# Kernel tuning notes

Hardware: AMD Instinct MI355X
Metric: run time of the kernel (lower is better)

Reference implementation:

```python
import jax, jax.numpy as jnp
import numpy as np


def setup_inputs() -> dict:
    key = jax.random.key(0)
    k1, k2 = jax.random.split(key)
    B, N = 2, 8192
    pred = jax.random.normal(k1, (B, N, 3), dtype=jnp.float32)
    gt = jax.random.normal(k2, (B, N, 3), dtype=jnp.float32)
    return {"pred": pred, "gt": gt}


def reference(pred, gt):
    # dist[b, i, j] = ||pred[b, j] - gt[b, i]||_2, computed via the
    # squared-norm expansion to avoid materializing a [B,N,N,3] diff tensor.
    p_sq = jnp.sum(pred * pred, axis=-1)  # [B, N]
    g_sq = jnp.sum(gt * gt, axis=-1)      # [B, N]
    # inner[b, i, j] = gt[b, i] . pred[b, j]
    inner = jnp.einsum("bid,bjd->bij", gt, pred)  # [B, N, N]
    sq_dist = g_sq[:, :, None] + p_sq[:, None, :] - 2.0 * inner
    dist = jnp.sqrt(jnp.maximum(sq_dist, 0.0))    # [B, N, N]
    dist1 = jnp.min(dist, axis=2)  # per-gt nearest pred distance, [B, N]
    dist2 = jnp.min(dist, axis=1)  # per-pred nearest gt distance, [B, N]
    chamfer = (dist1.mean(axis=1) + dist2.mean(axis=1)).mean()
    return chamfer
```

## Files before the change

kernel.cpp:

```cpp
#include <hip/hip_runtime.h>
#include <math.h>

#define NPTS   8192
#define BATCH  2
#define TPB    256
#define PPB    32
#define NBLK   (2 * BATCH * NPTS / PPB)
#define CHUNK  1024
#define NCHUNK (NPTS / CHUNK)
#define NSL    64
#define GPS    (CHUNK / NSL / 4)
#define SPAD   (GPS + 1)
#define KPT    (PPB / 4)
#define POISON 0xAAAAAAAAu
#define TARGET (POISON + (unsigned)NBLK - 1u)
#define SCALE  (1.0f / (float)(BATCH * NPTS))

typedef float v2f __attribute__((ext_vector_type(2)));
typedef float v4f __attribute__((ext_vector_type(4)));

__global__ __launch_bounds__(TPB, 2) void chamfer_fused(
    const float* __restrict__ pred, const float* __restrict__ gt,
    unsigned int* __restrict__ ws, float* __restrict__ out)
{
    __shared__ v4f S[4 * NSL * SPAD];
    __shared__ float psq_l[PPB];
    v4f* xs4 = S;
    v4f* ys4 = S + NSL * SPAD;
    v4f* zs4 = S + 2 * NSL * SPAD;
    v4f* qs4 = S + 3 * NSL * SPAD;

    const int tid = threadIdx.x;
    const int pg  = tid & 3;
    const int cs  = tid >> 2;

    const int base = blockIdx.x * PPB;
    const int dir  = base >> 14;
    const int b    = (base >> 13) & 1;
    const int i0   = base & (NPTS - 1);

    const float* pts  = (dir == 0 ? gt : pred) + (size_t)b * NPTS * 3;
    const float* cand = (dir == 0 ? pred : gt) + (size_t)b * NPTS * 3;

    float px[KPT], py[KPT], pz[KPT], m[KPT];
    {
        const v4f* p4 = (const v4f*)(pts + (size_t)(i0 + pg * KPT) * 3);
        v4f A0 = p4[0], A1 = p4[1], A2 = p4[2], A3 = p4[3], A4 = p4[4], A5 = p4[5];
        px[0] = A0.x; py[0] = A0.y; pz[0] = A0.z;
        px[1] = A0.w; py[1] = A1.x; pz[1] = A1.y;
        px[2] = A1.z; py[2] = A1.w; pz[2] = A2.x;
        px[3] = A2.y; py[3] = A2.z; pz[3] = A2.w;
        px[4] = A3.x; py[4] = A3.y; pz[4] = A3.z;
        px[5] = A3.w; py[5] = A4.x; pz[5] = A4.y;
        px[6] = A4.z; py[6] = A4.w; pz[6] = A5.x;
        px[7] = A5.y; py[7] = A5.z; pz[7] = A5.w;
#pragma unroll
        for (int k = 0; k < KPT; ++k) m[k] = 3.0e38f;
    }

    const v4f* cand4 = (const v4f*)cand;

    for (int c = 0; c < NCHUNK; ++c) {
        if (c) __syncthreads();
        {
            const v4f* cb = cand4 + (size_t)c * (CHUNK * 3 / 4);
            v4f a  = cb[tid * 3 + 0];
            v4f bb = cb[tid * 3 + 1];
            v4f cc = cb[tid * 3 + 2];
            v4f X = {a.x, a.w, bb.z, cc.y};
            v4f Y = {a.y, bb.x, bb.w, cc.z};
            v4f Z = {a.z, bb.y, cc.x, cc.w};
            v4f Q = 0.5f * (X * X + Y * Y + Z * Z);
            int idx = (tid >> 2) * SPAD + (tid & 3);
            xs4[idx] = X; ys4[idx] = Y; zs4[idx] = Z; qs4[idx] = Q;
        }
        __syncthreads();

#pragma unroll
        for (int g = 0; g < GPS; ++g) {
            int idx = cs * SPAD + g;
            v4f cx = xs4[idx], cy = ys4[idx], cz = zs4[idx], cq = qs4[idx];
            v2f cxa = cx.xy, cxb = cx.zw, cya = cy.xy, cyb = cy.zw;
            v2f cza = cz.xy, czb = cz.zw, cqa = cq.xy, cqb = cq.zw;
#pragma unroll
            for (int k = 0; k < KPT; ++k) {
                v2f ta = cqa - cxa * px[k];
                ta = ta - cya * py[k];
                ta = ta - cza * pz[k];
                v2f tb = cqb - cxb * px[k];
                tb = tb - cyb * py[k];
                tb = tb - czb * pz[k];
                m[k] = fminf(fminf(m[k], ta.x), ta.y);
                m[k] = fminf(fminf(m[k], tb.x), tb.y);
            }
        }
    }

    __syncthreads();
    float* pl = (float*)S;
#pragma unroll
    for (int k = 0; k < KPT; ++k)
        pl[(pg * KPT + k) * 68 + cs] = m[k];
    if (cs == 0) {
#pragma unroll
        for (int k = 0; k < KPT; ++k)
            psq_l[pg * KPT + k] = fmaf(px[k], px[k], fmaf(py[k], py[k], pz[k] * pz[k]));
    }
    __syncthreads();

    if (tid < PPB) {
        const v4f* pm4 = (const v4f*)pl;
        v4f mv = pm4[tid * 17];
#pragma unroll
        for (int j = 1; j < 16; ++j) {
            v4f t = pm4[tid * 17 + j];
            mv.x = fminf(mv.x, t.x); mv.y = fminf(mv.y, t.y);
            mv.z = fminf(mv.z, t.z); mv.w = fminf(mv.w, t.w);
        }
        float M = fminf(fminf(mv.x, mv.y), fminf(mv.z, mv.w));
        float d = sqrtf(fmaxf(fmaf(2.0f, M, psq_l[tid]), 0.0f));
#pragma unroll
        for (int off = 16; off > 0; off >>= 1) d += __shfl_down(d, off, 32);

        float* accum = (float*)ws;
        unsigned int* counter = ws + 2048;
        int last = 0;
        if (tid == 0) {
            atomicAdd(&accum[(blockIdx.x & 31) * 32], d * SCALE);
            __threadfence();
            unsigned int old = atomicAdd(counter, 1u);
            last = (old == TARGET) ? 1 : 0;
        }
        last = __shfl(last, 0, 32);
        if (last) {
            __threadfence();
            float s = atomicAdd(&accum[tid * 32], 0.0f);
#pragma unroll
            for (int off = 16; off > 0; off >>= 1) s += __shfl_down(s, off, 32);
            if (tid == 0) out[0] = s;
        }
    }
}

extern "C" void kernel_launch(void* const* d_in, const int* in_sizes, int n_in,
                              void* d_out, int out_size, void* d_ws, size_t ws_size,
                              hipStream_t stream) {
    const float* pred = (const float*)d_in[0];
    const float* gt   = (const float*)d_in[1];
    chamfer_fused<<<NBLK, TPB, 0, stream>>>(pred, gt, (unsigned int*)d_ws,
                                            (float*)d_out);
}
```

Baseline: 95.01 us.

## Precompute SoA candidate layout in a prepass and stream candidates from global memory

Adds a small prepass kernel that transposes pred and gt into structure-of-arrays form with a precomputed half squared norm. The main kernel then drops the LDS staging and its per-chunk barriers, reading candidate quads straight from global memory (L2/cache) in a partially unrolled loop. This removes the repeated per-block AoS-to-SoA conversion and the syncthreads overhead. In exchange it adds a second launch and relies on cache bandwidth instead of LDS, which could raise load latency in the inner loop.

```diff
diff --git a/kernel.cpp b/kernel.cpp
--- a/kernel.cpp
+++ b/kernel.cpp
@@ -6,29 +6,42 @@
 #define TPB    256
 #define PPB    32
 #define NBLK   (2 * BATCH * NPTS / PPB)
-#define CHUNK  1024
-#define NCHUNK (NPTS / CHUNK)
-#define NSL    64
-#define GPS    (CHUNK / NSL / 4)
-#define SPAD   (GPS + 1)
 #define KPT    (PPB / 4)
+#define NQUAD  (NPTS / 4)
+#define GPT    (NQUAD / 64)
 #define POISON 0xAAAAAAAAu
 #define TARGET (POISON + (unsigned)NBLK - 1u)
 #define SCALE  (1.0f / (float)(BATCH * NPTS))
+#define SOAOFF 4096
 
 typedef float v2f __attribute__((ext_vector_type(2)));
 typedef float v4f __attribute__((ext_vector_type(4)));
 
-__global__ __launch_bounds__(TPB, 2) void chamfer_fused(
+__global__ __launch_bounds__(TPB) void make_soa(
     const float* __restrict__ pred, const float* __restrict__ gt,
-    unsigned int* __restrict__ ws, float* __restrict__ out)
+    float* __restrict__ soa)
 {
-    __shared__ v4f S[4 * NSL * SPAD];
+    const int n = blockIdx.x * TPB + threadIdx.x;
+    const int s = n >> 11;
+    const int g = n & (NQUAD - 1);
+    const float* src = (s < 2) ? pred + (size_t)s * NPTS * 3
+                               : gt + (size_t)(s - 2) * NPTS * 3;
+    const v4f* s4 = (const v4f*)src;
+    v4f a = s4[g * 3 + 0], b = s4[g * 3 + 1], c = s4[g * 3 + 2];
+    v4f X = {a.x, a.w, b.z, c.y};
+    v4f Y = {a.y, b.x, b.w, c.z};
+    v4f Z = {a.z, b.y, c.x, c.w};
+    v4f Q = 0.5f * (X * X + Y * Y + Z * Z);
+    v4f* dst = (v4f*)(soa + (size_t)s * 4 * NPTS);
+    dst[g] = X; dst[NQUAD + g] = Y; dst[2 * NQUAD + g] = Z; dst[3 * NQUAD + g] = Q;
+}
+
+__global__ __launch_bounds__(TPB, 2) void chamfer_main(
+    const float* __restrict__ soa, unsigned int* __restrict__ ws,
+    float* __restrict__ out)
+{
+    __shared__ float pl[PPB * 68];
     __shared__ float psq_l[PPB];
-    v4f* xs4 = S;
-    v4f* ys4 = S + NSL * SPAD;
-    v4f* zs4 = S + 2 * NSL * SPAD;
-    v4f* qs4 = S + 3 * NSL * SPAD;
 
     const int tid = threadIdx.x;
     const int pg  = tid & 3;
@@ -39,65 +52,52 @@
     const int b    = (base >> 13) & 1;
     const int i0   = base & (NPTS - 1);
 
-    const float* pts  = (dir == 0 ? gt : pred) + (size_t)b * NPTS * 3;
-    const float* cand = (dir == 0 ? pred : gt) + (size_t)b * NPTS * 3;
+    const float* P = soa + (size_t)(dir == 0 ? 2 + b : b) * 4 * NPTS;
+    const float* C = soa + (size_t)(dir == 0 ? b : 2 + b) * 4 * NPTS;
 
     float px[KPT], py[KPT], pz[KPT], m[KPT];
     {
-        const v4f* p4 = (const v4f*)(pts + (size_t)(i0 + pg * KPT) * 3);
-        v4f A0 = p4[0], A1 = p4[1], A2 = p4[2], A3 = p4[3], A4 = p4[4], A5 = p4[5];
-        px[0] = A0.x; py[0] = A0.y; pz[0] = A0.z;
-        px[1] = A0.w; py[1] = A1.x; pz[1] = A1.y;
-        px[2] = A1.z; py[2] = A1.w; pz[2] = A2.x;
-        px[3] = A2.y; py[3] = A2.z; pz[3] = A2.w;
-        px[4] = A3.x; py[4] = A3.y; pz[4] = A3.z;
-        px[5] = A3.w; py[5] = A4.x; pz[5] = A4.y;
-        px[6] = A4.z; py[6] = A4.w; pz[6] = A5.x;
-        px[7] = A5.y; py[7] = A5.z; pz[7] = A5.w;
+        const int q0 = (i0 + pg * KPT) >> 2;
+        const v4f* Px = (const v4f*)P;
+        const v4f* Py = (const v4f*)(P + NPTS);
+        const v4f* Pz = (const v4f*)(P + 2 * NPTS);
+        v4f x0 = Px[q0], x1 = Px[q0 + 1];
+        v4f y0 = Py[q0], y1 = Py[q0 + 1];
+        v4f z0 = Pz[q0], z1 = Pz[q0 + 1];
+        px[0]=x0.x; px[1]=x0.y; px[2]=x0.z; px[3]=x0.w;
+        px[4]=x1.x; px[5]=x1.y; px[6]=x1.z; px[7]=x1.w;
+        py[0]=y0.x; py[1]=y0.y; py[2]=y0.z; py[3]=y0.w;
+        py[4]=y1.x; py[5]=y1.y; py[6]=y1.z; py[7]=y1.w;
+        pz[0]=z0.x; pz[1]=z0.y; pz[2]=z0.z; pz[3]=z0.w;
+        pz[4]=z1.x; pz[5]=z1.y; pz[6]=z1.z; pz[7]=z1.w;
 #pragma unroll
         for (int k = 0; k < KPT; ++k) m[k] = 3.0e38f;
     }
 
-    const v4f* cand4 = (const v4f*)cand;
+    const v4f* Cx = (const v4f*)C;
+    const v4f* Cy = (const v4f*)(C + NPTS);
+    const v4f* Cz = (const v4f*)(C + 2 * NPTS);
+    const v4f* Cq = (const v4f*)(C + 3 * NPTS);
 
-    for (int c = 0; c < NCHUNK; ++c) {
-        if (c) __syncthreads();
-        {
-            const v4f* cb = cand4 + (size_t)c * (CHUNK * 3 / 4);
-            v4f a  = cb[tid * 3 + 0];
-            v4f bb = cb[tid * 3 + 1];
-            v4f cc = cb[tid * 3 + 2];
-            v4f X = {a.x, a.w, bb.z, cc.y};
-            v4f Y = {a.y, bb.x, bb.w, cc.z};
-            v4f Z = {a.z, bb.y, cc.x, cc.w};
-            v4f Q = 0.5f * (X * X + Y * Y + Z * Z);
-            int idx = (tid >> 2) * SPAD + (tid & 3);
-            xs4[idx] = X; ys4[idx] = Y; zs4[idx] = Z; qs4[idx] = Q;
-        }
-        __syncthreads();
-
+#pragma unroll 4
+    for (int g = 0; g < GPT; ++g) {
+        const int qd = g * 64 + cs;
+        v4f cx = Cx[qd], cy = Cy[qd], cz = Cz[qd], cq = Cq[qd];
+        v2f cxa = cx.xy, cxb = cx.zw, cya = cy.xy, cyb = cy.zw;
+        v2f cza = cz.xy, czb = cz.zw, cqa = cq.xy, cqb = cq.zw;
 #pragma unroll
-        for (int g = 0; g < GPS; ++g) {
-            int idx = cs * SPAD + g;
-            v4f cx = xs4[idx], cy = ys4[idx], cz = zs4[idx], cq = qs4[idx];
-            v2f cxa = cx.xy, cxb = cx.zw, cya = cy.xy, cyb = cy.zw;
-            v2f cza = cz.xy, czb = cz.zw, cqa = cq.xy, cqb = cq.zw;
-#pragma unroll
-            for (int k = 0; k < KPT; ++k) {
-                v2f ta = cqa - cxa * px[k];
-                ta = ta - cya * py[k];
-                ta = ta - cza * pz[k];
-                v2f tb = cqb - cxb * px[k];
-                tb = tb - cyb * py[k];
-                tb = tb - czb * pz[k];
-                m[k] = fminf(fminf(m[k], ta.x), ta.y);
-                m[k] = fminf(fminf(m[k], tb.x), tb.y);
-            }
+        for (int k = 0; k < KPT; ++k) {
+            v2f ta = cqa - cxa * px[k];
+            ta = ta - cya * py[k];
+            ta = ta - cza * pz[k];
+            v2f tb = cqb - cxb * px[k];
+            tb = tb - cyb * py[k];
+            tb = tb - czb * pz[k];
+            m[k] = fminf(fminf(m[k], ta.x), ta.y);
+            m[k] = fminf(fminf(m[k], tb.x), tb.y);
         }
     }
 
-    __syncthreads();
-    float* pl = (float*)S;
 #pragma unroll
     for (int k = 0; k < KPT; ++k)
         pl[(pg * KPT + k) * 68 + cs] = m[k];
@@ -147,6 +147,9 @@
                               hipStream_t stream) {
     const float* pred = (const float*)d_in[0];
     const float* gt   = (const float*)d_in[1];
-    chamfer_fused<<<NBLK, TPB, 0, stream>>>(pred, gt, (unsigned int*)d_ws,
-                                            (float*)d_out);
+    float* soa = (float*)d_ws + SOAOFF;
+
+    make_soa<<<32, TPB, 0, stream>>>(pred, gt, soa);
+    chamfer_main<<<NBLK, TPB, 0, stream>>>(soa, (unsigned int*)d_ws,
+                                           (float*)d_out);
 }
```

Result: no change. 94.67 us (-0.4%).
